# Kernel optimization log

Measured on AMD Instinct MI355X. Metric: run time of the kernel, lower is better.

Reference implementation:

```python
import jax, jax.numpy as jnp
import numpy as np

EPS = 1e-5


def setup_inputs() -> dict:
    key = jax.random.key(0)
    k_u, k_v, k_w, k_g, k_b, k_m, k_var = jax.random.split(key, 7)
    B, S, C1, C2, H, W = 4, 8, 64, 64, 128, 128
    CC = C1 + C2  # concat channels = out channels = 128
    u = jax.random.normal(k_u, (B, 1, C1, H, W), dtype=jnp.float32)
    v = jax.random.normal(k_v, (B, S, C2, H, W), dtype=jnp.float32)
    conv_w = jax.random.normal(k_w, (CC, CC, 3, 3), dtype=jnp.float32) * 0.05  # OIHW
    bn_gamma = jnp.ones((CC,), jnp.float32) + 0.1 * jax.random.normal(k_g, (CC,), dtype=jnp.float32)
    bn_beta = 0.1 * jax.random.normal(k_b, (CC,), dtype=jnp.float32)
    bn_mean = 0.1 * jax.random.normal(k_m, (CC,), dtype=jnp.float32)
    bn_var = jnp.abs(jax.random.normal(k_var, (CC,), dtype=jnp.float32)) + 0.5
    return {"u": u, "v": v, "conv_w": conv_w, "bn_gamma": bn_gamma,
            "bn_beta": bn_beta, "bn_mean": bn_mean, "bn_var": bn_var}


def _cross_conv(u, v, conv_w, bn_gamma, bn_beta, bn_mean, bn_var):
    B, _, C1, H, W = u.shape
    _, S, C2, _, _ = v.shape
    # broadcast u over the s axis, concat channels -> (b*s, c1+c2, h, w)
    us = jnp.broadcast_to(u[:, 0, None], (B, S, C1, H, W))
    xy = jnp.concatenate([us, v], axis=2).reshape(B * S, C1 + C2, H, W)
    # 3x3 conv, stride 1, SAME padding, no bias (BN follows)
    y = jax.lax.conv_general_dilated(
        xy, conv_w, window_strides=(1, 1), padding=((1, 1), (1, 1)),
        dimension_numbers=("NCHW", "OIHW", "NCHW"))
    # BatchNorm (inference: running stats)
    scale = (bn_gamma * jax.lax.rsqrt(bn_var + EPS))[None, :, None, None]
    shift = (bn_beta - bn_mean * bn_gamma * jax.lax.rsqrt(bn_var + EPS))[None, :, None, None]
    y = y * scale + shift
    # skip = Identity (concat_channels == out_channels, stride 1), then ReLU
    out = jax.nn.relu(y + xy)
    return out.reshape(B, 1, S, C1 + C2, H, W)


def reference(u, v, conv_w, bn_gamma, bn_beta, bn_mean, bn_var):
    return _cross_conv(u, v, conv_w, bn_gamma, bn_beta, bn_mean, bn_var)
```

## Files before the change

kernel.cpp:

```cpp
#include <hip/hip_runtime.h>
#include <hip/hip_bf16.h>


#define EPS 1e-5f

typedef __attribute__((ext_vector_type(8))) short short8;
typedef __attribute__((ext_vector_type(4))) float f32x4;
typedef __attribute__((ext_vector_type(2))) float f32x2;

constexpr int C1 = 64, CC = 128, Hd = 128, Wd = 128;
constexpr int HW = Hd * Wd;
constexpr int SP = 18;
constexpr int ROW = 40;
constexpr int WFRAGS = 9 * 4 * 8;
constexpr int NTHR = 512;
constexpr int UNITS = 16 * 18 * 10;
constexpr int NU = (UNITS + NTHR - 1) / NTHR;

__global__ void prep_weights(const float* __restrict__ wgt, ushort* __restrict__ wf) {
    int idx = blockIdx.x * 256 + threadIdx.x;
    if (idx >= WFRAGS * 64) return;
    int l  = idx & 63;
    int f  = idx >> 6;
    int cf = f & 7;
    int c  = (f >> 3) & 3;
    int t  = f >> 5;
    int kh = t / 3, kw = t % 3;
    int co  = cf * 16 + (l & 15);
    int cib = c * 32 + (l >> 4) * 8;
    ushort* dst = wf + (size_t)idx * 8;
#pragma unroll
    for (int j = 0; j < 8; ++j) {
        float x = wgt[(((size_t)co * CC + cib + j) * 3 + kh) * 3 + kw];
        __hip_bfloat16 bb = __float2bfloat16(x);
        dst[j] = *(ushort*)&bb;
    }
}

__global__ __launch_bounds__(NTHR, 2)
void crossconv_mfma(const float* __restrict__ u,
                    const float* __restrict__ v,
                    const ushort* __restrict__ wf,
                    const float* __restrict__ gamma,
                    const float* __restrict__ beta,
                    const float* __restrict__ mean,
                    const float* __restrict__ var,
                    float* __restrict__ out) {
    __shared__ alignas(16) ushort in_s[2][SP * SP * ROW];
    __shared__ float s_sc[CC], s_sh[CC];

    const int tid = threadIdx.x;
    const int w0 = blockIdx.x * 16;
    const int h0 = blockIdx.y * 16;
    const int n  = blockIdx.z;
    const int b  = n >> 3;
    const float* __restrict__ ubase = u + (size_t)b * C1 * HW;
    const float* __restrict__ vbase = v + (size_t)n * C1 * HW;

    if (tid < CC) {
        float sc = gamma[tid] * rsqrtf(var[tid] + EPS);
        s_sc[tid] = sc;
        s_sh[tid] = beta[tid] - mean[tid] * sc;
    }
    {
        uint4 z{0u, 0u, 0u, 0u};
        uint4* p = (uint4*)&in_s[0][0];
        for (int i = tid; i < 2 * SP * SP * ROW * 2 / 16; i += NTHR) p[i] = z;
    }

    const int l = tid & 63, wid = tid >> 6;
    const int n16 = l & 15, kgrp = l >> 4;

    int  goff[NU];
    int  sidx[NU];
    uint lm = 0, m0 = 0, m1 = 0;
#pragma unroll
    for (int i = 0; i < NU; ++i) {
        goff[i] = 0; sidx[i] = ROW;
        int e = tid + i * NTHR;
        if (e < UNITS) {
            int cp  = e / 180;
            int r   = e - cp * 180;
            int sph = r / 10;
            int j   = r - sph * 10;
            int gh  = h0 + sph - 1;
            int gw  = w0 + 2 * j - 2;
            sidx[i] = (sph * SP + 2 * j) * ROW + 2 * cp;
            if ((unsigned)gh < (unsigned)Hd && (unsigned)gw < (unsigned)(Wd - 1)) {
                goff[i] = 2 * cp * HW + gh * Wd + gw;
                lm |= 1u << i;
                if (j >= 1) m0 |= 1u << i;
                if (j <= 8) m1 |= 1u << i;
            }
        }
    }

    f32x4 acc[8][2];
#pragma unroll
    for (int cf = 0; cf < 8; ++cf) { acc[cf][0] = (f32x4)0.f; acc[cf][1] = (f32x4)0.f; }

    f32x2 sa[NU], sb[NU];

    auto chunk_src = [&](int c) -> const float* {
        return (c < 2) ? ubase + (size_t)c * 32 * HW
                       : vbase + (size_t)(c - 2) * 32 * HW;
    };
    auto stage_load = [&](const float* __restrict__ src) {
#pragma unroll
        for (int i = 0; i < NU; ++i) {
            sa[i] = f32x2{0.f, 0.f}; sb[i] = f32x2{0.f, 0.f};
            if (lm & (1u << i)) {
                const float* p = src + goff[i];
                sa[i] = *(const f32x2*)p;
                sb[i] = *(const f32x2*)(p + HW);
            }
        }
    };
    auto stage_write = [&](int buf) {
        ushort* __restrict__ d = in_s[buf];
#pragma unroll
        for (int i = 0; i < NU; ++i) {
            __hip_bfloat16 ax = __float2bfloat16(sa[i].x);
            __hip_bfloat16 bx = __float2bfloat16(sb[i].x);
            __hip_bfloat16 ay = __float2bfloat16(sa[i].y);
            __hip_bfloat16 by = __float2bfloat16(sb[i].y);
            uint v0 = (uint)*(ushort*)&ax | ((uint)*(ushort*)&bx << 16);
            uint v1 = (uint)*(ushort*)&ay | ((uint)*(ushort*)&by << 16);
            if (m0 & (1u << i)) *(uint*)&d[sidx[i] - ROW] = v0;
            if (m1 & (1u << i)) *(uint*)&d[sidx[i]]       = v1;
        }
    };
    auto compute = [&](int buf, int c) {
        const ushort* __restrict__ bs = in_s[buf];
#pragma unroll
        for (int t = 0; t < 9; ++t) {
            const int kh = t / 3, kw = t % 3;
            const int spw = n16 + kw;
            short8 p0 = *(const short8*)&bs[((wid * 2 + 0 + kh) * SP + spw) * ROW + kgrp * 8];
            short8 p1 = *(const short8*)&bs[((wid * 2 + 1 + kh) * SP + spw) * ROW + kgrp * 8];
            const short8* __restrict__ wp =
                (const short8*)wf + ((size_t)(t * 4 + c) * 8) * 64 + l;
#pragma unroll
            for (int cf = 0; cf < 8; ++cf) {
                short8 wfr = wp[(size_t)cf * 64];
                acc[cf][0] = __builtin_amdgcn_mfma_f32_16x16x32_bf16(p0, wfr, acc[cf][0], 0, 0, 0);
                acc[cf][1] = __builtin_amdgcn_mfma_f32_16x16x32_bf16(p1, wfr, acc[cf][1], 0, 0, 0);
            }
        }
    };

    stage_load(chunk_src(0));
    __syncthreads();
    stage_write(0);
    __syncthreads();

    for (int c = 0; c < 4; ++c) {
        if (c < 3) stage_load(chunk_src(c + 1));
        compute(c & 1, c);
        if (c < 3) stage_write((c & 1) ^ 1);
        __syncthreads();
    }

#pragma unroll
    for (int cf = 0; cf < 8; ++cf) {
        const int co = cf * 16 + n16;
        const float sc = s_sc[co], sh = s_sh[co];
        const float* __restrict__ xb = (cf < 4) ? (ubase + (size_t)co * HW)
                                                : (vbase + (size_t)(co - C1) * HW);
        float* __restrict__ ob = out + ((size_t)n * CC + co) * HW;
#pragma unroll
        for (int pf = 0; pf < 2; ++pf) {
            const int off = (h0 + wid * 2 + pf) * Wd + w0 + kgrp * 4;
            f32x4 x = *(const f32x4*)(xb + off);
            f32x4 a = acc[cf][pf];
            f32x4 y;
#pragma unroll
            for (int r = 0; r < 4; ++r)
                y[r] = fmaxf(fmaf(a[r], sc, sh) + x[r], 0.f);
            *(f32x4*)(ob + off) = y;
        }
    }
}

extern "C" void kernel_launch(void* const* d_in, const int* in_sizes, int n_in,
                              void* d_out, int out_size, void* d_ws, size_t ws_size,
                              hipStream_t stream) {
    const float* u     = (const float*)d_in[0];
    const float* v     = (const float*)d_in[1];
    const float* wgt   = (const float*)d_in[2];
    const float* gamma = (const float*)d_in[3];
    const float* beta  = (const float*)d_in[4];
    const float* mean  = (const float*)d_in[5];
    const float* var   = (const float*)d_in[6];
    float* out = (float*)d_out;
    ushort* wf = (ushort*)d_ws;

    prep_weights<<<dim3((WFRAGS * 64 + 255) / 256), dim3(256), 0, stream>>>(wgt, wf);
    crossconv_mfma<<<dim3(Wd / 16, Hd / 16, 32), dim3(NTHR), 0, stream>>>(
        u, v, wf, gamma, beta, mean, var, out);
}
```

Baseline: 1.007 ms.

## Split output channels across waves and shrink spatial tile to 16x8

Each wave now computes 2 output-channel fragments over all 8 rows of a 16x8 tile, instead of all 8 channel fragments over 2 rows of a 16x16 tile. Per-tap global weight fragment loads per wave drop from 8 to 2, while LDS input reads rise from 2 to 8. Block size halves to 256 threads with occupancy hint 3, and the halo overhead of the smaller tile grows (10 rows staged for 8 output rows versus 18 for 16).

```diff
diff --git a/kernel.cpp b/kernel.cpp
--- a/kernel.cpp
+++ b/kernel.cpp
@@ -10,11 +10,12 @@
 
 constexpr int C1 = 64, CC = 128, Hd = 128, Wd = 128;
 constexpr int HW = Hd * Wd;
-constexpr int SP = 18;
+constexpr int TW = 16, TH = 8;
+constexpr int SPW = 18, SPH = 10;
 constexpr int ROW = 40;
 constexpr int WFRAGS = 9 * 4 * 8;
-constexpr int NTHR = 512;
-constexpr int UNITS = 16 * 18 * 10;
+constexpr int NTHR = 256;
+constexpr int UNITS = 16 * SPH * 10;
 constexpr int NU = (UNITS + NTHR - 1) / NTHR;
 
 __global__ void prep_weights(const float* __restrict__ wgt, ushort* __restrict__ wf) {
@@ -37,7 +38,7 @@
     }
 }
 
-__global__ __launch_bounds__(NTHR, 2)
+__global__ __launch_bounds__(NTHR, 3)
 void crossconv_mfma(const float* __restrict__ u,
                     const float* __restrict__ v,
                     const ushort* __restrict__ wf,
@@ -46,12 +47,12 @@
                     const float* __restrict__ mean,
                     const float* __restrict__ var,
                     float* __restrict__ out) {
-    __shared__ alignas(16) ushort in_s[2][SP * SP * ROW];
+    __shared__ alignas(16) ushort in_s[2][SPH * SPW * ROW];
     __shared__ float s_sc[CC], s_sh[CC];
 
     const int tid = threadIdx.x;
-    const int w0 = blockIdx.x * 16;
-    const int h0 = blockIdx.y * 16;
+    const int w0 = blockIdx.x * TW;
+    const int h0 = blockIdx.y * TH;
     const int n  = blockIdx.z;
     const int b  = n >> 3;
     const float* __restrict__ ubase = u + (size_t)b * C1 * HW;
@@ -65,7 +66,7 @@
     {
         uint4 z{0u, 0u, 0u, 0u};
         uint4* p = (uint4*)&in_s[0][0];
-        for (int i = tid; i < 2 * SP * SP * ROW * 2 / 16; i += NTHR) p[i] = z;
+        for (int i = tid; i < 2 * SPH * SPW * ROW * 2 / 16; i += NTHR) p[i] = z;
     }
 
     const int l = tid & 63, wid = tid >> 6;
@@ -79,13 +80,13 @@
         goff[i] = 0; sidx[i] = ROW;
         int e = tid + i * NTHR;
         if (e < UNITS) {
-            int cp  = e / 180;
-            int r   = e - cp * 180;
+            int cp  = e / 100;
+            int r   = e - cp * 100;
             int sph = r / 10;
             int j   = r - sph * 10;
             int gh  = h0 + sph - 1;
             int gw  = w0 + 2 * j - 2;
-            sidx[i] = (sph * SP + 2 * j) * ROW + 2 * cp;
+            sidx[i] = (sph * SPW + 2 * j) * ROW + 2 * cp;
             if ((unsigned)gh < (unsigned)Hd && (unsigned)gw < (unsigned)(Wd - 1)) {
                 goff[i] = 2 * cp * HW + gh * Wd + gw;
                 lm |= 1u << i;
@@ -95,9 +96,11 @@
         }
     }
 
-    f32x4 acc[8][2];
-#pragma unroll
-    for (int cf = 0; cf < 8; ++cf) { acc[cf][0] = (f32x4)0.f; acc[cf][1] = (f32x4)0.f; }
+    f32x4 acc[2][8];
+#pragma unroll
+    for (int cfl = 0; cfl < 2; ++cfl)
+#pragma unroll
+        for (int pf = 0; pf < 8; ++pf) acc[cfl][pf] = (f32x4)0.f;
 
     f32x2 sa[NU], sb[NU];
 
@@ -136,15 +139,15 @@
         for (int t = 0; t < 9; ++t) {
             const int kh = t / 3, kw = t % 3;
             const int spw = n16 + kw;
-            short8 p0 = *(const short8*)&bs[((wid * 2 + 0 + kh) * SP + spw) * ROW + kgrp * 8];
-            short8 p1 = *(const short8*)&bs[((wid * 2 + 1 + kh) * SP + spw) * ROW + kgrp * 8];
             const short8* __restrict__ wp =
-                (const short8*)wf + ((size_t)(t * 4 + c) * 8) * 64 + l;
-#pragma unroll
-            for (int cf = 0; cf < 8; ++cf) {
-                short8 wfr = wp[(size_t)cf * 64];
-                acc[cf][0] = __builtin_amdgcn_mfma_f32_16x16x32_bf16(p0, wfr, acc[cf][0], 0, 0, 0);
-                acc[cf][1] = __builtin_amdgcn_mfma_f32_16x16x32_bf16(p1, wfr, acc[cf][1], 0, 0, 0);
+                (const short8*)wf + ((size_t)((t * 4 + c) * 8 + wid * 2)) * 64 + l;
+            short8 wf0 = wp[0];
+            short8 wf1 = wp[64];
+#pragma unroll
+            for (int pf = 0; pf < 8; ++pf) {
+                short8 p = *(const short8*)&bs[((pf + kh) * SPW + spw) * ROW + kgrp * 8];
+                acc[0][pf] = __builtin_amdgcn_mfma_f32_16x16x32_bf16(p, wf0, acc[0][pf], 0, 0, 0);
+                acc[1][pf] = __builtin_amdgcn_mfma_f32_16x16x32_bf16(p, wf1, acc[1][pf], 0, 0, 0);
             }
         }
     };
@@ -154,6 +157,7 @@
     stage_write(0);
     __syncthreads();
 
+#pragma unroll
     for (int c = 0; c < 4; ++c) {
         if (c < 3) stage_load(chunk_src(c + 1));
         compute(c & 1, c);
@@ -162,17 +166,17 @@
     }
 
 #pragma unroll
-    for (int cf = 0; cf < 8; ++cf) {
-        const int co = cf * 16 + n16;
+    for (int cfl = 0; cfl < 2; ++cfl) {
+        const int co = (wid * 2 + cfl) * 16 + n16;
         const float sc = s_sc[co], sh = s_sh[co];
-        const float* __restrict__ xb = (cf < 4) ? (ubase + (size_t)co * HW)
-                                                : (vbase + (size_t)(co - C1) * HW);
+        const float* __restrict__ xb = (co < C1) ? (ubase + (size_t)co * HW)
+                                                 : (vbase + (size_t)(co - C1) * HW);
         float* __restrict__ ob = out + ((size_t)n * CC + co) * HW;
 #pragma unroll
-        for (int pf = 0; pf < 2; ++pf) {
-            const int off = (h0 + wid * 2 + pf) * Wd + w0 + kgrp * 4;
+        for (int pf = 0; pf < 8; ++pf) {
+            const int off = (h0 + pf) * Wd + w0 + kgrp * 4;
             f32x4 x = *(const f32x4*)(xb + off);
-            f32x4 a = acc[cf][pf];
+            f32x4 a = acc[cfl][pf];
             f32x4 y;
 #pragma unroll
             for (int r = 0; r < 4; ++r)
@@ -196,6 +200,6 @@
     ushort* wf = (ushort*)d_ws;
 
     prep_weights<<<dim3((WFRAGS * 64 + 255) / 256), dim3(256), 0, stream>>>(wgt, wf);
-    crossconv_mfma<<<dim3(Wd / 16, Hd / 16, 32), dim3(NTHR), 0, stream>>>(
+    crossconv_mfma<<<dim3(Wd / TW, Hd / TH, 32), dim3(NTHR), 0, stream>>>(
         u, v, wf, gamma, beta, mean, var, out);
 }
```

Result: faster. 929.7 us (-7.6%).
